# Performance work log

Measured on AMD Instinct MI355X. Metric: run time of the kernel, lower is better.

## Reference

```python
import jax, jax.numpy as jnp
import numpy as np

N_NODES = 50000
N_EDGES = 800000
N_GRAPHS = 64
IN_CH = 128
HID = [64, 128]
MLP_CH = [128, 64, 64, 64, 1]


def _glorot(key, fan_in, fan_out):
    lim = jnp.sqrt(6.0 / (fan_in + fan_out))
    return jax.random.uniform(key, (fan_in, fan_out), jnp.float32, -lim, lim)


def setup_inputs() -> dict:
    key = jax.random.key(0)
    ks = jax.random.split(key, 16)
    x = jax.random.normal(ks[0], (N_NODES, IN_CH), jnp.float32)
    edge_index = jax.random.randint(ks[1], (2, N_EDGES), 0, N_NODES, jnp.int64)
    batch = jnp.sort(jax.random.randint(ks[2], (N_NODES,), 0, N_GRAPHS, jnp.int64))
    inp = {"x": x, "edge_index": edge_index, "batch": batch}
    # GCNConv weights (x @ W + b)
    inp["W1"] = _glorot(ks[3], IN_CH, HID[0]);  inp["b1"] = jnp.zeros((HID[0],), jnp.float32)
    inp["W2"] = _glorot(ks[4], HID[0], HID[1]); inp["b2"] = jnp.zeros((HID[1],), jnp.float32)
    # MLP weights
    for i in range(4):
        inp[f"M{i+1}"] = _glorot(ks[5 + i], MLP_CH[i], MLP_CH[i + 1])
        inp[f"c{i+1}"] = jnp.zeros((MLP_CH[i + 1],), jnp.float32)
    return inp


def _gcn_conv(x, src, dst, dinv, W, b):
    # x' = D^-1/2 (A + I) D^-1/2 (x W) + b, via gather-scale-scatter over edges
    h = x @ W                                   # [N, F]
    norm = dinv[src] * dinv[dst]                # [E+N]
    msg = h[src] * norm[:, None]                # gather + scale
    out = jax.ops.segment_sum(msg, dst, num_segments=x.shape[0])
    return out + b


def reference(x, edge_index, batch, W1, b1, W2, b2, M1, c1, M2, c2, M3, c3, M4, c4):
    N = x.shape[0]
    x = x.astype(jnp.float32)
    # add self loops (PyG GCNConv default)
    loops = jnp.arange(N, dtype=edge_index.dtype)
    src = jnp.concatenate([edge_index[0], loops])
    dst = jnp.concatenate([edge_index[1], loops])
    deg = jax.ops.segment_sum(jnp.ones_like(src, jnp.float32), dst, num_segments=N)
    dinv = jnp.where(deg > 0, jax.lax.rsqrt(jnp.maximum(deg, 1.0)), 0.0)

    h = jax.nn.relu(_gcn_conv(x, src, dst, dinv, W1, b1))
    h = jax.nn.relu(_gcn_conv(h, src, dst, dinv, W2, b2))

    # global mean pool per graph
    sums = jax.ops.segment_sum(h, batch, num_segments=N_GRAPHS)
    cnts = jax.ops.segment_sum(jnp.ones((N,), jnp.float32), batch, num_segments=N_GRAPHS)
    g = sums / jnp.maximum(cnts, 1.0)[:, None]   # [G, 128]

    # MLP (eval mode: dropout is identity)
    g = jax.nn.leaky_relu(g @ M1 + c1, negative_slope=0.2)
    g = jax.nn.leaky_relu(g @ M2 + c2, negative_slope=0.1)
    g = jax.nn.leaky_relu(g @ M3 + c3, negative_slope=0.1)
    g = jax.nn.relu(g @ M4 + c4)
    return g
```

## Files before the change

kernel.cpp:

```cpp
#include <hip/hip_runtime.h>
#include <hip/hip_fp16.h>

#define N_NODES 50000
#define N_EDGES 800000
#define N_GRAPHS 64

#define CAP 64
#define FILL_STRIPES 256

struct __align__(8)  h4v { __half2 a, b; };
struct __align__(16) h8v { __half2 a, b, c, d; };


__global__ void k_zero_pack(int* __restrict__ cnt, float* __restrict__ sums,
                            const int* __restrict__ src, const int* __restrict__ dst,
                            unsigned* __restrict__ pk,
                            const float* __restrict__ W2, __half* __restrict__ w2h,
                            const int* __restrict__ batch, int* __restrict__ gend) {
    int i = blockIdx.x * 256 + threadIdx.x;
    if (i < N_NODES) {
        cnt[i] = 0;
        if (i == N_NODES - 1 || batch[i] != batch[i + 1]) gend[batch[i]] = i + 1;
    }
    if (i < N_GRAPHS * 128) sums[i] = 0.f;
    if (i < 64 * 128) w2h[i] = __float2half_rn(W2[i]);
    if (i < N_EDGES) pk[i] = ((unsigned)dst[i] << 16) | (unsigned)src[i];
}


__global__ void k_fill_direct(const unsigned* __restrict__ pk, int* __restrict__ cnt,
                              unsigned short* __restrict__ csr, int E) {
    const int range = blockIdx.x & 7;
    const int stripe = blockIdx.x >> 3;
    const unsigned lo = range * (N_NODES / 8);
    const unsigned hi = lo + (N_NODES / 8);
    for (int e = stripe * 256 + threadIdx.x; e < E; e += FILL_STRIPES * 256) {
        unsigned p = pk[e];
        unsigned d = p >> 16;
        if (d >= lo && d < hi) {
            int slot = atomicAdd(&cnt[d], 1);
            if (slot < CAP) csr[(size_t)d * CAP + slot] = (unsigned short)(p & 0xffffu);
        }
    }
}


__global__ __launch_bounds__(256) void k_gemm1(const float* __restrict__ A,
                                               const float* __restrict__ W,
                                               const int* __restrict__ cnt,
                                               __half* __restrict__ Cout, int N) {
    const int FIN = 128;
    __shared__ __align__(16) float As[64 * (FIN + 2)];
    __shared__ __align__(16) float Wsm[FIN * 64];
    const int t = threadIdx.x;
    const int row0 = blockIdx.x * 64;

    const int NF4 = 64 * FIN / 4;
    for (int idx = t; idx < NF4; idx += 256) {
        int r = idx / (FIN / 4);
        int c4 = idx % (FIN / 4);
        float4 v = make_float4(0.f, 0.f, 0.f, 0.f);
        if (row0 + r < N) v = ((const float4*)(A + (size_t)(row0 + r) * FIN))[c4];
        float* p = &As[r * (FIN + 2) + c4 * 4];
        ((float2*)p)[0] = make_float2(v.x, v.y);
        ((float2*)p)[1] = make_float2(v.z, v.w);
    }
    for (int idx = t; idx < FIN * 16; idx += 256) {
        int r = idx / 16, c4 = idx % 16;
        *((float4*)&Wsm[r * 64 + c4 * 4]) = ((const float4*)(W + (size_t)r * 64))[c4];
    }
    __syncthreads();

    const int tc = (t & 15) * 4;
    const int tr = (t >> 4) * 4;
    float acc[4][4] = {};
#pragma unroll 4
    for (int k = 0; k < FIN; k += 2) {
        float2 a[4];
#pragma unroll
        for (int r = 0; r < 4; ++r)
            a[r] = *(const float2*)&As[(tr + r) * (FIN + 2) + k];
        float4 w0 = *(const float4*)&Wsm[k * 64 + tc];
        float4 w1 = *(const float4*)&Wsm[(k + 1) * 64 + tc];
#pragma unroll
        for (int r = 0; r < 4; ++r) {
            acc[r][0] = fmaf(a[r].x, w0.x, acc[r][0]);
            acc[r][1] = fmaf(a[r].x, w0.y, acc[r][1]);
            acc[r][2] = fmaf(a[r].x, w0.z, acc[r][2]);
            acc[r][3] = fmaf(a[r].x, w0.w, acc[r][3]);
            acc[r][0] = fmaf(a[r].y, w1.x, acc[r][0]);
            acc[r][1] = fmaf(a[r].y, w1.y, acc[r][1]);
            acc[r][2] = fmaf(a[r].y, w1.z, acc[r][2]);
            acc[r][3] = fmaf(a[r].y, w1.w, acc[r][3]);
        }
    }

#pragma unroll
    for (int r = 0; r < 4; ++r) {
        int row = row0 + tr + r;
        if (row < N) {
            float s = rsqrtf((float)(min(cnt[row], CAP) + 1));
            __half2* dsth = (__half2*)(Cout + (size_t)row * 64 + tc);
            dsth[0] = __floats2half2_rn(acc[r][0] * s, acc[r][1] * s);
            dsth[1] = __floats2half2_rn(acc[r][2] * s, acc[r][3] * s);
        }
    }
}


template <bool RELU>
__global__ void k_agg(const h8v* __restrict__ h, const int* __restrict__ cnt,
                      const unsigned short* __restrict__ csr,
                      const float* __restrict__ bias, h8v* __restrict__ out, int N) {
    int node = blockIdx.x * 32 + (threadIdx.x >> 3);
    int lane = threadIdx.x & 7;
    if (node >= N) return;
    int c = min(cnt[node], CAP);
    float di = rsqrtf((float)(c + 1));
    h8v sv = h[(size_t)node * 8 + lane];
    float2 p0 = __half22float2(sv.a), p1 = __half22float2(sv.b);
    float2 p2 = __half22float2(sv.c), p3 = __half22float2(sv.d);
    float f0 = p0.x, f1 = p0.y, f2 = p1.x, f3 = p1.y;
    float f4 = p2.x, f5 = p2.y, f6 = p3.x, f7 = p3.y;
    float g0 = 0, g1 = 0, g2 = 0, g3 = 0, g4 = 0, g5 = 0, g6 = 0, g7 = 0;
    const unsigned short* row = csr + (size_t)node * CAP;
    int j = 0;
    for (; j + 4 <= c; j += 4) {
        ushort4 s4 = *(const ushort4*)(row + j);
        h8v v0 = h[(size_t)s4.x * 8 + lane];
        h8v v1 = h[(size_t)s4.y * 8 + lane];
        h8v v2 = h[(size_t)s4.z * 8 + lane];
        h8v v3 = h[(size_t)s4.w * 8 + lane];
        float2 a0 = __half22float2(v0.a), a1 = __half22float2(v0.b),
               a2 = __half22float2(v0.c), a3 = __half22float2(v0.d);
        float2 b0 = __half22float2(v1.a), b1 = __half22float2(v1.b),
               b2 = __half22float2(v1.c), b3 = __half22float2(v1.d);
        f0 += a0.x; f1 += a0.y; f2 += a1.x; f3 += a1.y;
        f4 += a2.x; f5 += a2.y; f6 += a3.x; f7 += a3.y;
        g0 += b0.x; g1 += b0.y; g2 += b1.x; g3 += b1.y;
        g4 += b2.x; g5 += b2.y; g6 += b3.x; g7 += b3.y;
        float2 c0 = __half22float2(v2.a), c1 = __half22float2(v2.b),
               c2 = __half22float2(v2.c), c3 = __half22float2(v2.d);
        float2 d0 = __half22float2(v3.a), d1 = __half22float2(v3.b),
               d2 = __half22float2(v3.c), d3 = __half22float2(v3.d);
        f0 += c0.x; f1 += c0.y; f2 += c1.x; f3 += c1.y;
        f4 += c2.x; f5 += c2.y; f6 += c3.x; f7 += c3.y;
        g0 += d0.x; g1 += d0.y; g2 += d1.x; g3 += d1.y;
        g4 += d2.x; g5 += d2.y; g6 += d3.x; g7 += d3.y;
    }
    for (; j < c; ++j) {
        h8v v = h[(size_t)row[j] * 8 + lane];
        float2 a0 = __half22float2(v.a), a1 = __half22float2(v.b),
               a2 = __half22float2(v.c), a3 = __half22float2(v.d);
        f0 += a0.x; f1 += a0.y; f2 += a1.x; f3 += a1.y;
        f4 += a2.x; f5 += a2.y; f6 += a3.x; f7 += a3.y;
    }
    float s0 = f0 + g0, s1 = f1 + g1, s2 = f2 + g2, s3 = f3 + g3;
    float s4 = f4 + g4, s5 = f5 + g5, s6 = f6 + g6, s7 = f7 + g7;
    h8v o;
    if (RELU) {
        float4 bv0 = ((const float4*)bias)[lane * 2];
        float4 bv1 = ((const float4*)bias)[lane * 2 + 1];
        float r0 = fmaf(s0, di, bv0.x); r0 = r0 > 0.f ? r0 : 0.f;
        float r1 = fmaf(s1, di, bv0.y); r1 = r1 > 0.f ? r1 : 0.f;
        float r2 = fmaf(s2, di, bv0.z); r2 = r2 > 0.f ? r2 : 0.f;
        float r3 = fmaf(s3, di, bv0.w); r3 = r3 > 0.f ? r3 : 0.f;
        float r4 = fmaf(s4, di, bv1.x); r4 = r4 > 0.f ? r4 : 0.f;
        float r5 = fmaf(s5, di, bv1.y); r5 = r5 > 0.f ? r5 : 0.f;
        float r6 = fmaf(s6, di, bv1.z); r6 = r6 > 0.f ? r6 : 0.f;
        float r7 = fmaf(s7, di, bv1.w); r7 = r7 > 0.f ? r7 : 0.f;
        o.a = __floats2half2_rn(di * r0, di * r1);
        o.b = __floats2half2_rn(di * r2, di * r3);
        o.c = __floats2half2_rn(di * r4, di * r5);
        o.d = __floats2half2_rn(di * r6, di * r7);
    } else {
        o.a = __floats2half2_rn(s0 * di, s1 * di);
        o.b = __floats2half2_rn(s2 * di, s3 * di);
        o.c = __floats2half2_rn(s4 * di, s5 * di);
        o.d = __floats2half2_rn(s6 * di, s7 * di);
    }
    out[(size_t)node * 8 + lane] = o;
}


__global__ __launch_bounds__(256) void k_gemm_pool128(
    const __half2* __restrict__ A2,
    const __half2* __restrict__ w2h,
    const float* __restrict__ bias,
    const int* __restrict__ batch,
    float* __restrict__ sums, int N) {
    __shared__ __align__(16) float As[64 * 66];
    __shared__ __align__(16) __half2 Wh[64 * 64];
    __shared__ float red[8][132];
    __shared__ int batchLDS[64];
    const int t = threadIdx.x;
    const int row0 = blockIdx.x * 64;

    for (int idx = t; idx < 4096; idx += 256) Wh[idx] = w2h[idx];
    if (t < 64) batchLDS[t] = batch[min(row0 + t, N - 1)];
    for (int idx = t; idx < 64 * 32; idx += 256) {
        int r = idx >> 5, c2 = idx & 31;
        float2 v = make_float2(0.f, 0.f);
        if (row0 + r < N) v = __half22float2(A2[(size_t)(row0 + r) * 32 + c2]);
        *(float2*)&As[r * 66 + c2 * 2] = v;
    }
    __syncthreads();

    const int tc = (t & 31) * 4;
    const int tr = (t >> 5) * 8;
    float acc[8][4] = {};
#pragma unroll 4
    for (int k = 0; k < 64; k += 2) {
        float2 a[8];
#pragma unroll
        for (int r = 0; r < 8; ++r)
            a[r] = *(const float2*)&As[(tr + r) * 66 + k];
        h4v wv0 = *(const h4v*)&Wh[k * 64 + (tc >> 1)];
        h4v wv1 = *(const h4v*)&Wh[(k + 1) * 64 + (tc >> 1)];
        float2 w00 = __half22float2(wv0.a), w01 = __half22float2(wv0.b);
        float2 w10 = __half22float2(wv1.a), w11 = __half22float2(wv1.b);
#pragma unroll
        for (int r = 0; r < 8; ++r) {
            acc[r][0] = fmaf(a[r].x, w00.x, acc[r][0]);
            acc[r][1] = fmaf(a[r].x, w00.y, acc[r][1]);
            acc[r][2] = fmaf(a[r].x, w01.x, acc[r][2]);
            acc[r][3] = fmaf(a[r].x, w01.y, acc[r][3]);
            acc[r][0] = fmaf(a[r].y, w10.x, acc[r][0]);
            acc[r][1] = fmaf(a[r].y, w10.y, acc[r][1]);
            acc[r][2] = fmaf(a[r].y, w11.x, acc[r][2]);
            acc[r][3] = fmaf(a[r].y, w11.y, acc[r][3]);
        }
    }

    float4 bv = *(const float4*)&bias[tc];
    float v[8][4];
#pragma unroll
    for (int r = 0; r < 8; ++r) {
        bool valid = (row0 + tr + r) < N;
        v[r][0] = valid ? fmaxf(acc[r][0] + bv.x, 0.f) : 0.f;
        v[r][1] = valid ? fmaxf(acc[r][1] + bv.y, 0.f) : 0.f;
        v[r][2] = valid ? fmaxf(acc[r][2] + bv.z, 0.f) : 0.f;
        v[r][3] = valid ? fmaxf(acc[r][3] + bv.w, 0.f) : 0.f;
    }

    const int g0 = batchLDS[0], g1 = batchLDS[63];
    const int rg = t >> 5;
    for (int g = g0; g <= g1; ++g) {
        float p0 = 0.f, p1 = 0.f, p2 = 0.f, p3 = 0.f;
#pragma unroll
        for (int r = 0; r < 8; ++r) {
            if (batchLDS[tr + r] == g) { p0 += v[r][0]; p1 += v[r][1]; p2 += v[r][2]; p3 += v[r][3]; }
        }
        red[rg][tc + 0] = p0; red[rg][tc + 1] = p1;
        red[rg][tc + 2] = p2; red[rg][tc + 3] = p3;
        __syncthreads();
        for (int off = 4; off > 0; off >>= 1) {
            if (rg < off) {
#pragma unroll
                for (int c = 0; c < 4; ++c) red[rg][tc + c] += red[rg + off][tc + c];
            }
            __syncthreads();
        }
        if (rg == 0) {
#pragma unroll
            for (int c = 0; c < 4; ++c)
                atomicAdd(&sums[g * 128 + tc + c], red[0][tc + c]);
        }
        __syncthreads();
    }
}


__global__ void k_mlp(const float* __restrict__ sums, const int* __restrict__ gend,
                      const float* __restrict__ M1, const float* __restrict__ c1,
                      const float* __restrict__ M2, const float* __restrict__ c2,
                      const float* __restrict__ M3, const float* __restrict__ c3,
                      const float* __restrict__ M4, const float* __restrict__ c4,
                      float* __restrict__ out) {
    __shared__ float g[128], t1[64], t2[64], t3[64];
    __shared__ float cntb;
    int b = blockIdx.x;
    int t = threadIdx.x;
    if (t == 0) {
        int lb = (b > 0) ? gend[b - 1] : 0;
        cntb = fmaxf((float)(gend[b] - lb), 1.0f);
    }
    __syncthreads();
    if (t < 128) g[t] = sums[b * 128 + t] / cntb;
    __syncthreads();
    if (t < 64) {
        float acc = c1[t];
        for (int k = 0; k < 128; ++k) acc = fmaf(g[k], M1[k * 64 + t], acc);
        t1[t] = acc >= 0.f ? acc : 0.2f * acc;
    }
    __syncthreads();
    if (t < 64) {
        float acc = c2[t];
        for (int k = 0; k < 64; ++k) acc = fmaf(t1[k], M2[k * 64 + t], acc);
        t2[t] = acc >= 0.f ? acc : 0.1f * acc;
    }
    __syncthreads();
    if (t < 64) {
        float acc = c3[t];
        for (int k = 0; k < 64; ++k) acc = fmaf(t2[k], M3[k * 64 + t], acc);
        t3[t] = acc >= 0.f ? acc : 0.1f * acc;
    }
    __syncthreads();
    if (t == 0) {
        float acc = c4[0];
        for (int k = 0; k < 64; ++k) acc = fmaf(t3[k], M4[k], acc);
        out[b] = fmaxf(acc, 0.f);
    }
}


extern "C" void kernel_launch(void* const* d_in, const int* in_sizes, int n_in,
                              void* d_out, int out_size, void* d_ws, size_t ws_size,
                              hipStream_t stream) {
    const float* x   = (const float*)d_in[0];
    const int*   ei  = (const int*)d_in[1];
    const int*   bat = (const int*)d_in[2];
    const float* W1  = (const float*)d_in[3];
    const float* b1  = (const float*)d_in[4];
    const float* W2  = (const float*)d_in[5];
    const float* b2  = (const float*)d_in[6];
    const float* M1  = (const float*)d_in[7];
    const float* c1  = (const float*)d_in[8];
    const float* M2  = (const float*)d_in[9];
    const float* c2  = (const float*)d_in[10];
    const float* M3  = (const float*)d_in[11];
    const float* c3  = (const float*)d_in[12];
    const float* M4  = (const float*)d_in[13];
    const float* c4  = (const float*)d_in[14];
    float* out = (float*)d_out;

    const int* src = ei;
    const int* dst = ei + N_EDGES;

    float* bufA    = (float*)d_ws;
    float* bufB    = bufA + (size_t)N_NODES * 64;
    float* sums    = bufB + (size_t)N_NODES * 64;
    int*   cnt     = (int*)(sums + N_GRAPHS * 128);
    unsigned short* csr = (unsigned short*)(cnt + N_NODES);
    unsigned* pk   = (unsigned*)(csr + (size_t)N_NODES * CAP);
    __half* w2h    = (__half*)(pk + N_EDGES);
    int*   gend    = (int*)(w2h + 64 * 128);

    k_zero_pack<<<(N_EDGES + 255) / 256, 256, 0, stream>>>(cnt, sums, src, dst, pk,
                                                           W2, w2h, bat, gend);
    k_fill_direct<<<8 * FILL_STRIPES, 256, 0, stream>>>(pk, cnt, csr, N_EDGES);

    const int NBLK = (N_NODES + 63) / 64;
    const int ABLK = (N_NODES + 31) / 32;

    k_gemm1<<<NBLK, 256, 0, stream>>>(x, W1, cnt, (__half*)bufA, N_NODES);
    k_agg<true><<<ABLK, 256, 0, stream>>>(
        (const h8v*)bufA, cnt, csr, b1, (h8v*)bufB, N_NODES);

    k_agg<false><<<ABLK, 256, 0, stream>>>(
        (const h8v*)bufB, cnt, csr, nullptr, (h8v*)bufA, N_NODES);
    k_gemm_pool128<<<NBLK, 256, 0, stream>>>(
        (const __half2*)bufA, (const __half2*)w2h, b2, bat, sums, N_NODES);

    k_mlp<<<N_GRAPHS, 128, 0, stream>>>(sums, gend,
                                        M1, c1, M2, c2, M3, c3, M4, c4, out);
}
```

Measured before the change: 217.0 us.

## Merge build and tail stages into cooperative kernels with grid syncs

Replaces the zero/pack and fill kernels with one cooperative kernel that zeroes counters, syncs the grid, then fills the CSR directly from src/dst without the packed edge array. The second aggregation, the GEMM-pool and the MLP are merged into one cooperative persistent kernel with grid-wide syncs between phases. This aims to cut kernel launch gaps and the extra pack pass, in exchange for grid-sync cost, fewer resident blocks and less parallelism in some phases. The tail kernel's shared-memory use may limit how many blocks can be co-resident.

New measurement: 520.8 us. +140.0%, slower.

```diff
diff --git a/kernel.cpp b/kernel.cpp
--- a/kernel.cpp
+++ b/kernel.cpp
@@ -1,45 +1,46 @@
 #include <hip/hip_runtime.h>
 #include <hip/hip_fp16.h>
+#include <hip/hip_cooperative_groups.h>
+
+namespace cg = cooperative_groups;
 
 #define N_NODES 50000
 #define N_EDGES 800000
 #define N_GRAPHS 64
 
 #define CAP 64
-#define FILL_STRIPES 256
+#define BUILD_BLOCKS 1024
+#define TAIL_BLOCKS 1024
 
 struct __align__(8)  h4v { __half2 a, b; };
 struct __align__(16) h8v { __half2 a, b, c, d; };
 
 
-__global__ void k_zero_pack(int* __restrict__ cnt, float* __restrict__ sums,
-                            const int* __restrict__ src, const int* __restrict__ dst,
-                            unsigned* __restrict__ pk,
-                            const float* __restrict__ W2, __half* __restrict__ w2h,
-                            const int* __restrict__ batch, int* __restrict__ gend) {
-    int i = blockIdx.x * 256 + threadIdx.x;
-    if (i < N_NODES) {
-        cnt[i] = 0;
-        if (i == N_NODES - 1 || batch[i] != batch[i + 1]) gend[batch[i]] = i + 1;
-    }
-    if (i < N_GRAPHS * 128) sums[i] = 0.f;
-    if (i < 64 * 128) w2h[i] = __float2half_rn(W2[i]);
-    if (i < N_EDGES) pk[i] = ((unsigned)dst[i] << 16) | (unsigned)src[i];
-}
-
-
-__global__ void k_fill_direct(const unsigned* __restrict__ pk, int* __restrict__ cnt,
-                              unsigned short* __restrict__ csr, int E) {
+__global__ __launch_bounds__(256, 4) void k_build(
+    const int* __restrict__ src, const int* __restrict__ dst,
+    int* __restrict__ cnt, float* __restrict__ sums,
+    const float* __restrict__ W2, __half* __restrict__ w2h,
+    const int* __restrict__ batch, int* __restrict__ gend,
+    unsigned short* __restrict__ csr) {
+    const int tid = blockIdx.x * 256 + threadIdx.x;
+    if (tid < N_NODES) {
+        cnt[tid] = 0;
+        if (tid == N_NODES - 1 || batch[tid] != batch[tid + 1]) gend[batch[tid]] = tid + 1;
+    }
+    if (tid < N_GRAPHS * 128) sums[tid] = 0.f;
+    if (tid < 64 * 128) w2h[tid] = __float2half_rn(W2[tid]);
+
+    cg::this_grid().sync();
+
     const int range = blockIdx.x & 7;
     const int stripe = blockIdx.x >> 3;
-    const unsigned lo = range * (N_NODES / 8);
-    const unsigned hi = lo + (N_NODES / 8);
-    for (int e = stripe * 256 + threadIdx.x; e < E; e += FILL_STRIPES * 256) {
-        unsigned p = pk[e];
-        unsigned d = p >> 16;
+    const int lo = range * (N_NODES / 8);
+    const int hi = lo + (N_NODES / 8);
+    for (int e = stripe * 256 + threadIdx.x; e < N_EDGES; e += (BUILD_BLOCKS / 8) * 256) {
+        int d = dst[e];
         if (d >= lo && d < hi) {
             int slot = atomicAdd(&cnt[d], 1);
-            if (slot < CAP) csr[(size_t)d * CAP + slot] = (unsigned short)(p & 0xffffu);
+            if (slot < CAP) csr[(size_t)d * CAP + slot] = (unsigned short)src[e];
         }
     }
 }
@@ -108,22 +109,11 @@
 }
 
 
-template <bool RELU>
-__global__ void k_agg(const h8v* __restrict__ h, const int* __restrict__ cnt,
-                      const unsigned short* __restrict__ csr,
-                      const float* __restrict__ bias, h8v* __restrict__ out, int N) {
-    int node = blockIdx.x * 32 + (threadIdx.x >> 3);
-    int lane = threadIdx.x & 7;
-    if (node >= N) return;
-    int c = min(cnt[node], CAP);
-    float di = rsqrtf((float)(c + 1));
-    h8v sv = h[(size_t)node * 8 + lane];
-    float2 p0 = __half22float2(sv.a), p1 = __half22float2(sv.b);
-    float2 p2 = __half22float2(sv.c), p3 = __half22float2(sv.d);
-    float f0 = p0.x, f1 = p0.y, f2 = p1.x, f3 = p1.y;
-    float f4 = p2.x, f5 = p2.y, f6 = p3.x, f7 = p3.y;
+__device__ __forceinline__ void gather_node(const h8v* __restrict__ h,
+                                            const unsigned short* __restrict__ row,
+                                            int c, int lane,
+                                            float* f ) {
     float g0 = 0, g1 = 0, g2 = 0, g3 = 0, g4 = 0, g5 = 0, g6 = 0, g7 = 0;
-    const unsigned short* row = csr + (size_t)node * CAP;
     int j = 0;
     for (; j + 4 <= c; j += 4) {
         ushort4 s4 = *(const ushort4*)(row + j);
@@ -135,16 +125,16 @@
                a2 = __half22float2(v0.c), a3 = __half22float2(v0.d);
         float2 b0 = __half22float2(v1.a), b1 = __half22float2(v1.b),
                b2 = __half22float2(v1.c), b3 = __half22float2(v1.d);
-        f0 += a0.x; f1 += a0.y; f2 += a1.x; f3 += a1.y;
-        f4 += a2.x; f5 += a2.y; f6 += a3.x; f7 += a3.y;
+        f[0] += a0.x; f[1] += a0.y; f[2] += a1.x; f[3] += a1.y;
+        f[4] += a2.x; f[5] += a2.y; f[6] += a3.x; f[7] += a3.y;
         g0 += b0.x; g1 += b0.y; g2 += b1.x; g3 += b1.y;
         g4 += b2.x; g5 += b2.y; g6 += b3.x; g7 += b3.y;
         float2 c0 = __half22float2(v2.a), c1 = __half22float2(v2.b),
                c2 = __half22float2(v2.c), c3 = __half22float2(v2.d);
         float2 d0 = __half22float2(v3.a), d1 = __half22float2(v3.b),
                d2 = __half22float2(v3.c), d3 = __half22float2(v3.d);
-        f0 += c0.x; f1 += c0.y; f2 += c1.x; f3 += c1.y;
-        f4 += c2.x; f5 += c2.y; f6 += c3.x; f7 += c3.y;
+        f[0] += c0.x; f[1] += c0.y; f[2] += c1.x; f[3] += c1.y;
+        f[4] += c2.x; f[5] += c2.y; f[6] += c3.x; f[7] += c3.y;
         g0 += d0.x; g1 += d0.y; g2 += d1.x; g3 += d1.y;
         g4 += d2.x; g5 += d2.y; g6 += d3.x; g7 += d3.y;
     }
@@ -152,164 +142,206 @@
         h8v v = h[(size_t)row[j] * 8 + lane];
         float2 a0 = __half22float2(v.a), a1 = __half22float2(v.b),
                a2 = __half22float2(v.c), a3 = __half22float2(v.d);
-        f0 += a0.x; f1 += a0.y; f2 += a1.x; f3 += a1.y;
-        f4 += a2.x; f5 += a2.y; f6 += a3.x; f7 += a3.y;
-    }
-    float s0 = f0 + g0, s1 = f1 + g1, s2 = f2 + g2, s3 = f3 + g3;
-    float s4 = f4 + g4, s5 = f5 + g5, s6 = f6 + g6, s7 = f7 + g7;
+        f[0] += a0.x; f[1] += a0.y; f[2] += a1.x; f[3] += a1.y;
+        f[4] += a2.x; f[5] += a2.y; f[6] += a3.x; f[7] += a3.y;
+    }
+    f[0] += g0; f[1] += g1; f[2] += g2; f[3] += g3;
+    f[4] += g4; f[5] += g5; f[6] += g6; f[7] += g7;
+}
+
+
+__global__ void k_agg1(const h8v* __restrict__ h, const int* __restrict__ cnt,
+                       const unsigned short* __restrict__ csr,
+                       const float* __restrict__ bias, h8v* __restrict__ out, int N) {
+    int node = blockIdx.x * 32 + (threadIdx.x >> 3);
+    int lane = threadIdx.x & 7;
+    if (node >= N) return;
+    int c = min(cnt[node], CAP);
+    float di = rsqrtf((float)(c + 1));
+    h8v sv = h[(size_t)node * 8 + lane];
+    float2 p0 = __half22float2(sv.a), p1 = __half22float2(sv.b);
+    float2 p2 = __half22float2(sv.c), p3 = __half22float2(sv.d);
+    float f[8] = {p0.x, p0.y, p1.x, p1.y, p2.x, p2.y, p3.x, p3.y};
+    gather_node(h, csr + (size_t)node * CAP, c, lane, f);
+    float4 bv0 = ((const float4*)bias)[lane * 2];
+    float4 bv1 = ((const float4*)bias)[lane * 2 + 1];
+    float r0 = fmaf(f[0], di, bv0.x); r0 = r0 > 0.f ? r0 : 0.f;
+    float r1 = fmaf(f[1], di, bv0.y); r1 = r1 > 0.f ? r1 : 0.f;
+    float r2 = fmaf(f[2], di, bv0.z); r2 = r2 > 0.f ? r2 : 0.f;
+    float r3 = fmaf(f[3], di, bv0.w); r3 = r3 > 0.f ? r3 : 0.f;
+    float r4 = fmaf(f[4], di, bv1.x); r4 = r4 > 0.f ? r4 : 0.f;
+    float r5 = fmaf(f[5], di, bv1.y); r5 = r5 > 0.f ? r5 : 0.f;
+    float r6 = fmaf(f[6], di, bv1.z); r6 = r6 > 0.f ? r6 : 0.f;
+    float r7 = fmaf(f[7], di, bv1.w); r7 = r7 > 0.f ? r7 : 0.f;
     h8v o;
-    if (RELU) {
-        float4 bv0 = ((const float4*)bias)[lane * 2];
-        float4 bv1 = ((const float4*)bias)[lane * 2 + 1];
-        float r0 = fmaf(s0, di, bv0.x); r0 = r0 > 0.f ? r0 : 0.f;
-        float r1 = fmaf(s1, di, bv0.y); r1 = r1 > 0.f ? r1 : 0.f;
-        float r2 = fmaf(s2, di, bv0.z); r2 = r2 > 0.f ? r2 : 0.f;
-        float r3 = fmaf(s3, di, bv0.w); r3 = r3 > 0.f ? r3 : 0.f;
-        float r4 = fmaf(s4, di, bv1.x); r4 = r4 > 0.f ? r4 : 0.f;
-        float r5 = fmaf(s5, di, bv1.y); r5 = r5 > 0.f ? r5 : 0.f;
-        float r6 = fmaf(s6, di, bv1.z); r6 = r6 > 0.f ? r6 : 0.f;
-        float r7 = fmaf(s7, di, bv1.w); r7 = r7 > 0.f ? r7 : 0.f;
-        o.a = __floats2half2_rn(di * r0, di * r1);
-        o.b = __floats2half2_rn(di * r2, di * r3);
-        o.c = __floats2half2_rn(di * r4, di * r5);
-        o.d = __floats2half2_rn(di * r6, di * r7);
-    } else {
-        o.a = __floats2half2_rn(s0 * di, s1 * di);
-        o.b = __floats2half2_rn(s2 * di, s3 * di);
-        o.c = __floats2half2_rn(s4 * di, s5 * di);
-        o.d = __floats2half2_rn(s6 * di, s7 * di);
-    }
+    o.a = __floats2half2_rn(di * r0, di * r1);
+    o.b = __floats2half2_rn(di * r2, di * r3);
+    o.c = __floats2half2_rn(di * r4, di * r5);
+    o.d = __floats2half2_rn(di * r6, di * r7);
     out[(size_t)node * 8 + lane] = o;
 }
 
 
-__global__ __launch_bounds__(256) void k_gemm_pool128(
-    const __half2* __restrict__ A2,
+__global__ __launch_bounds__(256, 4) void k_tail(
+    const h8v* __restrict__ hB,
+    const int* __restrict__ cnt,
+    const unsigned short* __restrict__ csr,
+    h8v* __restrict__ zA,
     const __half2* __restrict__ w2h,
-    const float* __restrict__ bias,
+    const float* __restrict__ b2,
     const int* __restrict__ batch,
-    float* __restrict__ sums, int N) {
+    float* __restrict__ sums,
+    const int* __restrict__ gend,
+    const float* __restrict__ M1, const float* __restrict__ c1,
+    const float* __restrict__ M2, const float* __restrict__ c2,
+    const float* __restrict__ M3, const float* __restrict__ c3,
+    const float* __restrict__ M4, const float* __restrict__ c4,
+    float* __restrict__ out) {
     __shared__ __align__(16) float As[64 * 66];
     __shared__ __align__(16) __half2 Wh[64 * 64];
     __shared__ float red[8][132];
     __shared__ int batchLDS[64];
+    __shared__ float gv[128], t1[64], t2[64], t3[64];
+    __shared__ float cntb;
     const int t = threadIdx.x;
-    const int row0 = blockIdx.x * 64;
-
-    for (int idx = t; idx < 4096; idx += 256) Wh[idx] = w2h[idx];
-    if (t < 64) batchLDS[t] = batch[min(row0 + t, N - 1)];
-    for (int idx = t; idx < 64 * 32; idx += 256) {
-        int r = idx >> 5, c2 = idx & 31;
-        float2 v = make_float2(0.f, 0.f);
-        if (row0 + r < N) v = __half22float2(A2[(size_t)(row0 + r) * 32 + c2]);
-        *(float2*)&As[r * 66 + c2 * 2] = v;
-    }
-    __syncthreads();
-
-    const int tc = (t & 31) * 4;
-    const int tr = (t >> 5) * 8;
-    float acc[8][4] = {};
+    const int N = N_NODES;
+
+    {
+        const int lane = t & 7;
+        const int grp = t >> 3;
+        for (int base = blockIdx.x * 32; base < N; base += TAIL_BLOCKS * 32) {
+            int node = base + grp;
+            if (node < N) {
+                int c = min(cnt[node], CAP);
+                float di = rsqrtf((float)(c + 1));
+                h8v sv = hB[(size_t)node * 8 + lane];
+                float2 p0 = __half22float2(sv.a), p1 = __half22float2(sv.b);
+                float2 p2 = __half22float2(sv.c), p3 = __half22float2(sv.d);
+                float f[8] = {p0.x, p0.y, p1.x, p1.y, p2.x, p2.y, p3.x, p3.y};
+                gather_node(hB, csr + (size_t)node * CAP, c, lane, f);
+                h8v o;
+                o.a = __floats2half2_rn(f[0] * di, f[1] * di);
+                o.b = __floats2half2_rn(f[2] * di, f[3] * di);
+                o.c = __floats2half2_rn(f[4] * di, f[5] * di);
+                o.d = __floats2half2_rn(f[6] * di, f[7] * di);
+                zA[(size_t)node * 8 + lane] = o;
+            }
+        }
+    }
+
+    cg::this_grid().sync();
+
+    const __half2* A2 = (const __half2*)zA;
+    for (int row0 = blockIdx.x * 64; row0 < N; row0 += TAIL_BLOCKS * 64) {
+        for (int idx = t; idx < 4096; idx += 256) Wh[idx] = w2h[idx];
+        if (t < 64) batchLDS[t] = batch[min(row0 + t, N - 1)];
+        for (int idx = t; idx < 64 * 32; idx += 256) {
+            int r = idx >> 5, c2 = idx & 31;
+            float2 v = make_float2(0.f, 0.f);
+            if (row0 + r < N) v = __half22float2(A2[(size_t)(row0 + r) * 32 + c2]);
+            *(float2*)&As[r * 66 + c2 * 2] = v;
+        }
+        __syncthreads();
+
+        const int tc = (t & 31) * 4;
+        const int tr = (t >> 5) * 8;
+        float acc[8][4] = {};
 #pragma unroll 4
-    for (int k = 0; k < 64; k += 2) {
-        float2 a[8];
-#pragma unroll
-        for (int r = 0; r < 8; ++r)
-            a[r] = *(const float2*)&As[(tr + r) * 66 + k];
-        h4v wv0 = *(const h4v*)&Wh[k * 64 + (tc >> 1)];
-        h4v wv1 = *(const h4v*)&Wh[(k + 1) * 64 + (tc >> 1)];
-        float2 w00 = __half22float2(wv0.a), w01 = __half22float2(wv0.b);
-        float2 w10 = __half22float2(wv1.a), w11 = __half22float2(wv1.b);
+        for (int k = 0; k < 64; k += 2) {
+            float2 a[8];
+#pragma unroll
+            for (int r = 0; r < 8; ++r)
+                a[r] = *(const float2*)&As[(tr + r) * 66 + k];
+            h4v wv0 = *(const h4v*)&Wh[k * 64 + (tc >> 1)];
+            h4v wv1 = *(const h4v*)&Wh[(k + 1) * 64 + (tc >> 1)];
+            float2 w00 = __half22float2(wv0.a), w01 = __half22float2(wv0.b);
+            float2 w10 = __half22float2(wv1.a), w11 = __half22float2(wv1.b);
+#pragma unroll
+            for (int r = 0; r < 8; ++r) {
+                acc[r][0] = fmaf(a[r].x, w00.x, acc[r][0]);
+                acc[r][1] = fmaf(a[r].x, w00.y, acc[r][1]);
+                acc[r][2] = fmaf(a[r].x, w01.x, acc[r][2]);
+                acc[r][3] = fmaf(a[r].x, w01.y, acc[r][3]);
+                acc[r][0] = fmaf(a[r].y, w10.x, acc[r][0]);
+                acc[r][1] = fmaf(a[r].y, w10.y, acc[r][1]);
+                acc[r][2] = fmaf(a[r].y, w11.x, acc[r][2]);
+                acc[r][3] = fmaf(a[r].y, w11.y, acc[r][3]);
+            }
+        }
+
+        float4 bv = *(const float4*)&b2[tc];
+        float v[8][4];
 #pragma unroll
         for (int r = 0; r < 8; ++r) {
-            acc[r][0] = fmaf(a[r].x, w00.x, acc[r][0]);
-            acc[r][1] = fmaf(a[r].x, w00.y, acc[r][1]);
-            acc[r][2] = fmaf(a[r].x, w01.x, acc[r][2]);
-            acc[r][3] = fmaf(a[r].x, w01.y, acc[r][3]);
-            acc[r][0] = fmaf(a[r].y, w10.x, acc[r][0]);
-            acc[r][1] = fmaf(a[r].y, w10.y, acc[r][1]);
-            acc[r][2] = fmaf(a[r].y, w11.x, acc[r][2]);
-            acc[r][3] = fmaf(a[r].y, w11.y, acc[r][3]);
-        }
-    }
-
-    float4 bv = *(const float4*)&bias[tc];
-    float v[8][4];
-#pragma unroll
-    for (int r = 0; r < 8; ++r) {
-        bool valid = (row0 + tr + r) < N;
-        v[r][0] = valid ? fmaxf(acc[r][0] + bv.x, 0.f) : 0.f;
-        v[r][1] = valid ? fmaxf(acc[r][1] + bv.y, 0.f) : 0.f;
-        v[r][2] = valid ? fmaxf(acc[r][2] + bv.z, 0.f) : 0.f;
-        v[r][3] = valid ? fmaxf(acc[r][3] + bv.w, 0.f) : 0.f;
-    }
-
-    const int g0 = batchLDS[0], g1 = batchLDS[63];
-    const int rg = t >> 5;
-    for (int g = g0; g <= g1; ++g) {
-        float p0 = 0.f, p1 = 0.f, p2 = 0.f, p3 = 0.f;
-#pragma unroll
-        for (int r = 0; r < 8; ++r) {
-            if (batchLDS[tr + r] == g) { p0 += v[r][0]; p1 += v[r][1]; p2 += v[r][2]; p3 += v[r][3]; }
-        }
-        red[rg][tc + 0] = p0; red[rg][tc + 1] = p1;
-        red[rg][tc + 2] = p2; red[rg][tc + 3] = p3;
-        __syncthreads();
-        for (int off = 4; off > 0; off >>= 1) {
-            if (rg < off) {
-#pragma unroll
-                for (int c = 0; c < 4; ++c) red[rg][tc + c] += red[rg + off][tc + c];
+            bool valid = (row0 + tr + r) < N;
+            v[r][0] = valid ? fmaxf(acc[r][0] + bv.x, 0.f) : 0.f;
+            v[r][1] = valid ? fmaxf(acc[r][1] + bv.y, 0.f) : 0.f;
+            v[r][2] = valid ? fmaxf(acc[r][2] + bv.z, 0.f) : 0.f;
+            v[r][3] = valid ? fmaxf(acc[r][3] + bv.w, 0.f) : 0.f;
+        }
+
+        const int g0 = batchLDS[0], g1 = batchLDS[63];
+        const int rg = t >> 5;
+        for (int g = g0; g <= g1; ++g) {
+            float p0 = 0.f, p1 = 0.f, p2 = 0.f, p3 = 0.f;
+#pragma unroll
+            for (int r = 0; r < 8; ++r) {
+                if (batchLDS[tr + r] == g) { p0 += v[r][0]; p1 += v[r][1]; p2 += v[r][2]; p3 += v[r][3]; }
+            }
+            red[rg][tc + 0] = p0; red[rg][tc + 1] = p1;
+            red[rg][tc + 2] = p2; red[rg][tc + 3] = p3;
+            __syncthreads();
+            for (int off = 4; off > 0; off >>= 1) {
+                if (rg < off) {
+#pragma unroll
+                    for (int c = 0; c < 4; ++c) red[rg][tc + c] += red[rg + off][tc + c];
+                }
+                __syncthreads();
+            }
+            if (rg == 0) {
+#pragma unroll
+                for (int c = 0; c < 4; ++c)
+                    atomicAdd(&sums[g * 128 + tc + c], red[0][tc + c]);
             }
             __syncthreads();
         }
-        if (rg == 0) {
-#pragma unroll
-            for (int c = 0; c < 4; ++c)
-                atomicAdd(&sums[g * 128 + tc + c], red[0][tc + c]);
-        }
-        __syncthreads();
-    }
-}
-
-
-__global__ void k_mlp(const float* __restrict__ sums, const int* __restrict__ gend,
-                      const float* __restrict__ M1, const float* __restrict__ c1,
-                      const float* __restrict__ M2, const float* __restrict__ c2,
-                      const float* __restrict__ M3, const float* __restrict__ c3,
-                      const float* __restrict__ M4, const float* __restrict__ c4,
-                      float* __restrict__ out) {
-    __shared__ float g[128], t1[64], t2[64], t3[64];
-    __shared__ float cntb;
-    int b = blockIdx.x;
-    int t = threadIdx.x;
-    if (t == 0) {
-        int lb = (b > 0) ? gend[b - 1] : 0;
-        cntb = fmaxf((float)(gend[b] - lb), 1.0f);
-    }
-    __syncthreads();
-    if (t < 128) g[t] = sums[b * 128 + t] / cntb;
-    __syncthreads();
-    if (t < 64) {
-        float acc = c1[t];
-        for (int k = 0; k < 128; ++k) acc = fmaf(g[k], M1[k * 64 + t], acc);
-        t1[t] = acc >= 0.f ? acc : 0.2f * acc;
-    }
-    __syncthreads();
-    if (t < 64) {
-        float acc = c2[t];
-        for (int k = 0; k < 64; ++k) acc = fmaf(t1[k], M2[k * 64 + t], acc);
-        t2[t] = acc >= 0.f ? acc : 0.1f * acc;
-    }
-    __syncthreads();
-    if (t < 64) {
-        float acc = c3[t];
-        for (int k = 0; k < 64; ++k) acc = fmaf(t2[k], M3[k * 64 + t], acc);
-        t3[t] = acc >= 0.f ? acc : 0.1f * acc;
-    }
-    __syncthreads();
-    if (t == 0) {
-        float acc = c4[0];
-        for (int k = 0; k < 64; ++k) acc = fmaf(t3[k], M4[k], acc);
-        out[b] = fmaxf(acc, 0.f);
+        __syncthreads();
+    }
+
+    cg::this_grid().sync();
+
+    if (blockIdx.x < N_GRAPHS) {
+        int b = blockIdx.x;
+        if (t == 0) {
+            int lb = (b > 0) ? gend[b - 1] : 0;
+            cntb = fmaxf((float)(gend[b] - lb), 1.0f);
+        }
+        __syncthreads();
+        if (t < 128) gv[t] = sums[b * 128 + t] / cntb;
+        __syncthreads();
+        if (t < 64) {
+            float acc = c1[t];
+            for (int k = 0; k < 128; ++k) acc = fmaf(gv[k], M1[k * 64 + t], acc);
+            t1[t] = acc >= 0.f ? acc : 0.2f * acc;
+        }
+        __syncthreads();
+        if (t < 64) {
+            float acc = c2[t];
+            for (int k = 0; k < 64; ++k) acc = fmaf(t1[k], M2[k * 64 + t], acc);
+            t2[t] = acc >= 0.f ? acc : 0.1f * acc;
+        }
+        __syncthreads();
+        if (t < 64) {
+            float acc = c3[t];
+            for (int k = 0; k < 64; ++k) acc = fmaf(t2[k], M3[k * 64 + t], acc);
+            t3[t] = acc >= 0.f ? acc : 0.1f * acc;
+        }
+        __syncthreads();
+        if (t == 0) {
+            float acc = c4[0];
+            for (int k = 0; k < 64; ++k) acc = fmaf(t3[k], M4[k], acc);
+            out[b] = fmaxf(acc, 0.f);
+        }
     }
 }
 
@@ -342,26 +374,32 @@
     float* sums    = bufB + (size_t)N_NODES * 64;
     int*   cnt     = (int*)(sums + N_GRAPHS * 128);
     unsigned short* csr = (unsigned short*)(cnt + N_NODES);
-    unsigned* pk   = (unsigned*)(csr + (size_t)N_NODES * CAP);
-    __half* w2h    = (__half*)(pk + N_EDGES);
+    __half* w2h    = (__half*)(csr + (size_t)N_NODES * CAP);
     int*   gend    = (int*)(w2h + 64 * 128);
 
-    k_zero_pack<<<(N_EDGES + 255) / 256, 256, 0, stream>>>(cnt, sums, src, dst, pk,
-                                                           W2, w2h, bat, gend);
-    k_fill_direct<<<8 * FILL_STRIPES, 256, 0, stream>>>(pk, cnt, csr, N_EDGES);
+    {
+        void* args[] = {(void*)&src, (void*)&dst, (void*)&cnt, (void*)&sums,
+                        (void*)&W2, (void*)&w2h, (void*)&bat, (void*)&gend, (void*)&csr};
+        hipLaunchCooperativeKernel((const void*)k_build, dim3(BUILD_BLOCKS), dim3(256),
+                                   args, 0, stream);
+    }
 
     const int NBLK = (N_NODES + 63) / 64;
     const int ABLK = (N_NODES + 31) / 32;
 
     k_gemm1<<<NBLK, 256, 0, stream>>>(x, W1, cnt, (__half*)bufA, N_NODES);
-    k_agg<true><<<ABLK, 256, 0, stream>>>(
+    k_agg1<<<ABLK, 256, 0, stream>>>(
         (const h8v*)bufA, cnt, csr, b1, (h8v*)bufB, N_NODES);
 
-    k_agg<false><<<ABLK, 256, 0, stream>>>(
-        (const h8v*)bufB, cnt, csr, nullptr, (h8v*)bufA, N_NODES);
-    k_gemm_pool128<<<NBLK, 256, 0, stream>>>(
-        (const __half2*)bufA, (const __half2*)w2h, b2, bat, sums, N_NODES);
-
-    k_mlp<<<N_GRAPHS, 128, 0, stream>>>(sums, gend,
-                                        M1, c1, M2, c2, M3, c3, M4, c4, out);
-}
+    {
+        const h8v* hB = (const h8v*)bufB;
+        h8v* zA = (h8v*)bufA;
+        const __half2* w2h2 = (const __half2*)w2h;
+        void* args[] = {(void*)&hB, (void*)&cnt, (void*)&csr, (void*)&zA, (void*)&w2h2,
+                        (void*)&b2, (void*)&bat, (void*)&sums, (void*)&gend,
+                        (void*)&M1, (void*)&c1, (void*)&M2, (void*)&c2,
+                        (void*)&M3, (void*)&c3, (void*)&M4, (void*)&c4, (void*)&out};
+        hipLaunchCooperativeKernel((const void*)k_tail, dim3(TAIL_BLOCKS), dim3(256),
+                                   args, 0, stream);
+    }
+}
```

## Fuse MLP into pooling kernel via last-block pattern and drop edge packing

Applied to the files above, without the earlier changes.

The separate edge-packing pass is removed: the fill kernel now reads src/dst directly instead of a packed 32-bit array, and the init kernel shrinks to node-sized launches. The MLP kernel is folded into the pooling GEMM kernel: each block increments a done counter, and the last block to finish runs the four-layer MLP for all 64 graphs using a tiled register GEMM. This removes one launch plus the pack kernel's reads and writes, but fill reads two arrays per edge and the MLP runs serially on a single block at the tail.

Result: slower. 287.5 us (+32.4%).

```diff
diff --git a/kernel.cpp b/kernel.cpp
--- a/kernel.cpp
+++ b/kernel.cpp
@@ -12,34 +12,32 @@
 struct __align__(16) h8v { __half2 a, b, c, d; };
 
 
-__global__ void k_zero_pack(int* __restrict__ cnt, float* __restrict__ sums,
-                            const int* __restrict__ src, const int* __restrict__ dst,
-                            unsigned* __restrict__ pk,
-                            const float* __restrict__ W2, __half* __restrict__ w2h,
-                            const int* __restrict__ batch, int* __restrict__ gend) {
+__global__ void k_init(int* __restrict__ cnt, float* __restrict__ sums,
+                       const float* __restrict__ W2, __half* __restrict__ w2h,
+                       const int* __restrict__ batch, int* __restrict__ gend,
+                       int* __restrict__ done) {
     int i = blockIdx.x * 256 + threadIdx.x;
+    if (i == 0) *done = 0;
     if (i < N_NODES) {
         cnt[i] = 0;
         if (i == N_NODES - 1 || batch[i] != batch[i + 1]) gend[batch[i]] = i + 1;
     }
     if (i < N_GRAPHS * 128) sums[i] = 0.f;
     if (i < 64 * 128) w2h[i] = __float2half_rn(W2[i]);
-    if (i < N_EDGES) pk[i] = ((unsigned)dst[i] << 16) | (unsigned)src[i];
-}
-
-
-__global__ void k_fill_direct(const unsigned* __restrict__ pk, int* __restrict__ cnt,
-                              unsigned short* __restrict__ csr, int E) {
+}
+
+
+__global__ void k_fill_direct(const int* __restrict__ src, const int* __restrict__ dst,
+                              int* __restrict__ cnt, unsigned short* __restrict__ csr, int E) {
     const int range = blockIdx.x & 7;
     const int stripe = blockIdx.x >> 3;
-    const unsigned lo = range * (N_NODES / 8);
-    const unsigned hi = lo + (N_NODES / 8);
+    const int lo = range * (N_NODES / 8);
+    const int hi = lo + (N_NODES / 8);
     for (int e = stripe * 256 + threadIdx.x; e < E; e += FILL_STRIPES * 256) {
-        unsigned p = pk[e];
-        unsigned d = p >> 16;
+        int d = dst[e];
         if (d >= lo && d < hi) {
             int slot = atomicAdd(&cnt[d], 1);
-            if (slot < CAP) csr[(size_t)d * CAP + slot] = (unsigned short)(p & 0xffffu);
+            if (slot < CAP) csr[(size_t)d * CAP + slot] = (unsigned short)src[e];
         }
     }
 }
@@ -188,11 +186,19 @@
     const __half2* __restrict__ w2h,
     const float* __restrict__ bias,
     const int* __restrict__ batch,
-    float* __restrict__ sums, int N) {
-    __shared__ __align__(16) float As[64 * 66];
-    __shared__ __align__(16) __half2 Wh[64 * 64];
+    float* __restrict__ sums, int N,
+    int* __restrict__ done, const int* __restrict__ gend,
+    const float* __restrict__ M1, const float* __restrict__ c1,
+    const float* __restrict__ M2, const float* __restrict__ c2,
+    const float* __restrict__ M3, const float* __restrict__ c3,
+    const float* __restrict__ M4, const float* __restrict__ c4,
+    float* __restrict__ out) {
+    __shared__ __align__(16) unsigned char smem[33280];
     __shared__ float red[8][132];
     __shared__ int batchLDS[64];
+    __shared__ bool amLast;
+    float* As = (float*)smem;
+    __half2* Wh = (__half2*)(smem + 16896);
     const int t = threadIdx.x;
     const int row0 = blockIdx.x * 64;
 
@@ -208,108 +214,176 @@
 
     const int tc = (t & 31) * 4;
     const int tr = (t >> 5) * 8;
-    float acc[8][4] = {};
+    {
+        float acc[8][4] = {};
 #pragma unroll 4
-    for (int k = 0; k < 64; k += 2) {
-        float2 a[8];
-#pragma unroll
-        for (int r = 0; r < 8; ++r)
-            a[r] = *(const float2*)&As[(tr + r) * 66 + k];
-        h4v wv0 = *(const h4v*)&Wh[k * 64 + (tc >> 1)];
-        h4v wv1 = *(const h4v*)&Wh[(k + 1) * 64 + (tc >> 1)];
-        float2 w00 = __half22float2(wv0.a), w01 = __half22float2(wv0.b);
-        float2 w10 = __half22float2(wv1.a), w11 = __half22float2(wv1.b);
+        for (int k = 0; k < 64; k += 2) {
+            float2 a[8];
+#pragma unroll
+            for (int r = 0; r < 8; ++r)
+                a[r] = *(const float2*)&As[(tr + r) * 66 + k];
+            h4v wv0 = *(const h4v*)&Wh[k * 64 + (tc >> 1)];
+            h4v wv1 = *(const h4v*)&Wh[(k + 1) * 64 + (tc >> 1)];
+            float2 w00 = __half22float2(wv0.a), w01 = __half22float2(wv0.b);
+            float2 w10 = __half22float2(wv1.a), w11 = __half22float2(wv1.b);
+#pragma unroll
+            for (int r = 0; r < 8; ++r) {
+                acc[r][0] = fmaf(a[r].x, w00.x, acc[r][0]);
+                acc[r][1] = fmaf(a[r].x, w00.y, acc[r][1]);
+                acc[r][2] = fmaf(a[r].x, w01.x, acc[r][2]);
+                acc[r][3] = fmaf(a[r].x, w01.y, acc[r][3]);
+                acc[r][0] = fmaf(a[r].y, w10.x, acc[r][0]);
+                acc[r][1] = fmaf(a[r].y, w10.y, acc[r][1]);
+                acc[r][2] = fmaf(a[r].y, w11.x, acc[r][2]);
+                acc[r][3] = fmaf(a[r].y, w11.y, acc[r][3]);
+            }
+        }
+
+        float4 bv = *(const float4*)&bias[tc];
+        float v[8][4];
 #pragma unroll
         for (int r = 0; r < 8; ++r) {
-            acc[r][0] = fmaf(a[r].x, w00.x, acc[r][0]);
-            acc[r][1] = fmaf(a[r].x, w00.y, acc[r][1]);
-            acc[r][2] = fmaf(a[r].x, w01.x, acc[r][2]);
-            acc[r][3] = fmaf(a[r].x, w01.y, acc[r][3]);
-            acc[r][0] = fmaf(a[r].y, w10.x, acc[r][0]);
-            acc[r][1] = fmaf(a[r].y, w10.y, acc[r][1]);
-            acc[r][2] = fmaf(a[r].y, w11.x, acc[r][2]);
-            acc[r][3] = fmaf(a[r].y, w11.y, acc[r][3]);
-        }
-    }
-
-    float4 bv = *(const float4*)&bias[tc];
-    float v[8][4];
-#pragma unroll
-    for (int r = 0; r < 8; ++r) {
-        bool valid = (row0 + tr + r) < N;
-        v[r][0] = valid ? fmaxf(acc[r][0] + bv.x, 0.f) : 0.f;
-        v[r][1] = valid ? fmaxf(acc[r][1] + bv.y, 0.f) : 0.f;
-        v[r][2] = valid ? fmaxf(acc[r][2] + bv.z, 0.f) : 0.f;
-        v[r][3] = valid ? fmaxf(acc[r][3] + bv.w, 0.f) : 0.f;
-    }
-
-    const int g0 = batchLDS[0], g1 = batchLDS[63];
-    const int rg = t >> 5;
-    for (int g = g0; g <= g1; ++g) {
-        float p0 = 0.f, p1 = 0.f, p2 = 0.f, p3 = 0.f;
-#pragma unroll
-        for (int r = 0; r < 8; ++r) {
-            if (batchLDS[tr + r] == g) { p0 += v[r][0]; p1 += v[r][1]; p2 += v[r][2]; p3 += v[r][3]; }
-        }
-        red[rg][tc + 0] = p0; red[rg][tc + 1] = p1;
-        red[rg][tc + 2] = p2; red[rg][tc + 3] = p3;
-        __syncthreads();
-        for (int off = 4; off > 0; off >>= 1) {
-            if (rg < off) {
-#pragma unroll
-                for (int c = 0; c < 4; ++c) red[rg][tc + c] += red[rg + off][tc + c];
+            bool valid = (row0 + tr + r) < N;
+            v[r][0] = valid ? fmaxf(acc[r][0] + bv.x, 0.f) : 0.f;
+            v[r][1] = valid ? fmaxf(acc[r][1] + bv.y, 0.f) : 0.f;
+            v[r][2] = valid ? fmaxf(acc[r][2] + bv.z, 0.f) : 0.f;
+            v[r][3] = valid ? fmaxf(acc[r][3] + bv.w, 0.f) : 0.f;
+        }
+
+        const int g0 = batchLDS[0], g1 = batchLDS[63];
+        const int rg = t >> 5;
+        for (int g = g0; g <= g1; ++g) {
+            float p0 = 0.f, p1 = 0.f, p2 = 0.f, p3 = 0.f;
+#pragma unroll
+            for (int r = 0; r < 8; ++r) {
+                if (batchLDS[tr + r] == g) { p0 += v[r][0]; p1 += v[r][1]; p2 += v[r][2]; p3 += v[r][3]; }
+            }
+            red[rg][tc + 0] = p0; red[rg][tc + 1] = p1;
+            red[rg][tc + 2] = p2; red[rg][tc + 3] = p3;
+            __syncthreads();
+            for (int off = 4; off > 0; off >>= 1) {
+                if (rg < off) {
+#pragma unroll
+                    for (int c = 0; c < 4; ++c) red[rg][tc + c] += red[rg + off][tc + c];
+                }
+                __syncthreads();
+            }
+            if (rg == 0) {
+#pragma unroll
+                for (int c = 0; c < 4; ++c)
+                    atomicAdd(&sums[g * 128 + tc + c], red[0][tc + c]);
             }
             __syncthreads();
         }
-        if (rg == 0) {
-#pragma unroll
-            for (int c = 0; c < 4; ++c)
-                atomicAdd(&sums[g * 128 + tc + c], red[0][tc + c]);
-        }
+    }
+
+    __threadfence();
+    __syncthreads();
+    if (t == 0) amLast = (atomicAdd(done, 1) == (int)gridDim.x - 1);
+    __syncthreads();
+    if (!amLast) return;
+    __threadfence();
+
+    float* G = (float*)smem;
+    for (int idx = t; idx < N_GRAPHS * 128; idx += 256) {
+        int g = idx >> 7;
+        int lb = (g > 0) ? gend[g - 1] : 0;
+        float cg = fmaxf((float)(gend[g] - lb), 1.0f);
+        G[idx] = atomicAdd(&sums[idx], 0.f) / cg;
+    }
+    __syncthreads();
+
+    const int mc = (t & 15) * 4;
+    const int mr = (t >> 4) * 4;
+    float* T1 = (float*)smem;
+    float* T2 = (float*)(smem + 16384);
+    {
+        float acc[4][4] = {};
+        for (int k = 0; k < 128; ++k) {
+            float4 w = *(const float4*)&M1[k * 64 + mc];
+            float a0 = G[(mr + 0) * 128 + k], a1 = G[(mr + 1) * 128 + k];
+            float a2 = G[(mr + 2) * 128 + k], a3 = G[(mr + 3) * 128 + k];
+            acc[0][0] = fmaf(a0, w.x, acc[0][0]); acc[0][1] = fmaf(a0, w.y, acc[0][1]);
+            acc[0][2] = fmaf(a0, w.z, acc[0][2]); acc[0][3] = fmaf(a0, w.w, acc[0][3]);
+            acc[1][0] = fmaf(a1, w.x, acc[1][0]); acc[1][1] = fmaf(a1, w.y, acc[1][1]);
+            acc[1][2] = fmaf(a1, w.z, acc[1][2]); acc[1][3] = fmaf(a1, w.w, acc[1][3]);
+            acc[2][0] = fmaf(a2, w.x, acc[2][0]); acc[2][1] = fmaf(a2, w.y, acc[2][1]);
+            acc[2][2] = fmaf(a2, w.z, acc[2][2]); acc[2][3] = fmaf(a2, w.w, acc[2][3]);
+            acc[3][0] = fmaf(a3, w.x, acc[3][0]); acc[3][1] = fmaf(a3, w.y, acc[3][1]);
+            acc[3][2] = fmaf(a3, w.z, acc[3][2]); acc[3][3] = fmaf(a3, w.w, acc[3][3]);
+        }
+        float4 cv = *(const float4*)&c1[mc];
         __syncthreads();
-    }
-}
-
-
-__global__ void k_mlp(const float* __restrict__ sums, const int* __restrict__ gend,
-                      const float* __restrict__ M1, const float* __restrict__ c1,
-                      const float* __restrict__ M2, const float* __restrict__ c2,
-                      const float* __restrict__ M3, const float* __restrict__ c3,
-                      const float* __restrict__ M4, const float* __restrict__ c4,
-                      float* __restrict__ out) {
-    __shared__ float g[128], t1[64], t2[64], t3[64];
-    __shared__ float cntb;
-    int b = blockIdx.x;
-    int t = threadIdx.x;
-    if (t == 0) {
-        int lb = (b > 0) ? gend[b - 1] : 0;
-        cntb = fmaxf((float)(gend[b] - lb), 1.0f);
-    }
-    __syncthreads();
-    if (t < 128) g[t] = sums[b * 128 + t] / cntb;
-    __syncthreads();
-    if (t < 64) {
-        float acc = c1[t];
-        for (int k = 0; k < 128; ++k) acc = fmaf(g[k], M1[k * 64 + t], acc);
-        t1[t] = acc >= 0.f ? acc : 0.2f * acc;
-    }
-    __syncthreads();
-    if (t < 64) {
-        float acc = c2[t];
-        for (int k = 0; k < 64; ++k) acc = fmaf(t1[k], M2[k * 64 + t], acc);
-        t2[t] = acc >= 0.f ? acc : 0.1f * acc;
-    }
-    __syncthreads();
-    if (t < 64) {
-        float acc = c3[t];
-        for (int k = 0; k < 64; ++k) acc = fmaf(t2[k], M3[k * 64 + t], acc);
-        t3[t] = acc >= 0.f ? acc : 0.1f * acc;
-    }
-    __syncthreads();
-    if (t == 0) {
+#pragma unroll
+        for (int r = 0; r < 4; ++r) {
+            float o0 = acc[r][0] + cv.x, o1 = acc[r][1] + cv.y;
+            float o2 = acc[r][2] + cv.z, o3 = acc[r][3] + cv.w;
+            T1[(mr + r) * 64 + mc + 0] = o0 >= 0.f ? o0 : 0.2f * o0;
+            T1[(mr + r) * 64 + mc + 1] = o1 >= 0.f ? o1 : 0.2f * o1;
+            T1[(mr + r) * 64 + mc + 2] = o2 >= 0.f ? o2 : 0.2f * o2;
+            T1[(mr + r) * 64 + mc + 3] = o3 >= 0.f ? o3 : 0.2f * o3;
+        }
+    }
+    __syncthreads();
+    {
+        float acc[4][4] = {};
+        for (int k = 0; k < 64; ++k) {
+            float4 w = *(const float4*)&M2[k * 64 + mc];
+            float a0 = T1[(mr + 0) * 64 + k], a1 = T1[(mr + 1) * 64 + k];
+            float a2 = T1[(mr + 2) * 64 + k], a3 = T1[(mr + 3) * 64 + k];
+            acc[0][0] = fmaf(a0, w.x, acc[0][0]); acc[0][1] = fmaf(a0, w.y, acc[0][1]);
+            acc[0][2] = fmaf(a0, w.z, acc[0][2]); acc[0][3] = fmaf(a0, w.w, acc[0][3]);
+            acc[1][0] = fmaf(a1, w.x, acc[1][0]); acc[1][1] = fmaf(a1, w.y, acc[1][1]);
+            acc[1][2] = fmaf(a1, w.z, acc[1][2]); acc[1][3] = fmaf(a1, w.w, acc[1][3]);
+            acc[2][0] = fmaf(a2, w.x, acc[2][0]); acc[2][1] = fmaf(a2, w.y, acc[2][1]);
+            acc[2][2] = fmaf(a2, w.z, acc[2][2]); acc[2][3] = fmaf(a2, w.w, acc[2][3]);
+            acc[3][0] = fmaf(a3, w.x, acc[3][0]); acc[3][1] = fmaf(a3, w.y, acc[3][1]);
+            acc[3][2] = fmaf(a3, w.z, acc[3][2]); acc[3][3] = fmaf(a3, w.w, acc[3][3]);
+        }
+        float4 cv = *(const float4*)&c2[mc];
+#pragma unroll
+        for (int r = 0; r < 4; ++r) {
+            float o0 = acc[r][0] + cv.x, o1 = acc[r][1] + cv.y;
+            float o2 = acc[r][2] + cv.z, o3 = acc[r][3] + cv.w;
+            T2[(mr + r) * 64 + mc + 0] = o0 >= 0.f ? o0 : 0.1f * o0;
+            T2[(mr + r) * 64 + mc + 1] = o1 >= 0.f ? o1 : 0.1f * o1;
+            T2[(mr + r) * 64 + mc + 2] = o2 >= 0.f ? o2 : 0.1f * o2;
+            T2[(mr + r) * 64 + mc + 3] = o3 >= 0.f ? o3 : 0.1f * o3;
+        }
+    }
+    __syncthreads();
+    {
+        float acc[4][4] = {};
+        for (int k = 0; k < 64; ++k) {
+            float4 w = *(const float4*)&M3[k * 64 + mc];
+            float a0 = T2[(mr + 0) * 64 + k], a1 = T2[(mr + 1) * 64 + k];
+            float a2 = T2[(mr + 2) * 64 + k], a3 = T2[(mr + 3) * 64 + k];
+            acc[0][0] = fmaf(a0, w.x, acc[0][0]); acc[0][1] = fmaf(a0, w.y, acc[0][1]);
+            acc[0][2] = fmaf(a0, w.z, acc[0][2]); acc[0][3] = fmaf(a0, w.w, acc[0][3]);
+            acc[1][0] = fmaf(a1, w.x, acc[1][0]); acc[1][1] = fmaf(a1, w.y, acc[1][1]);
+            acc[1][2] = fmaf(a1, w.z, acc[1][2]); acc[1][3] = fmaf(a1, w.w, acc[1][3]);
+            acc[2][0] = fmaf(a2, w.x, acc[2][0]); acc[2][1] = fmaf(a2, w.y, acc[2][1]);
+            acc[2][2] = fmaf(a2, w.z, acc[2][2]); acc[2][3] = fmaf(a2, w.w, acc[2][3]);
+            acc[3][0] = fmaf(a3, w.x, acc[3][0]); acc[3][1] = fmaf(a3, w.y, acc[3][1]);
+            acc[3][2] = fmaf(a3, w.z, acc[3][2]); acc[3][3] = fmaf(a3, w.w, acc[3][3]);
+        }
+        float4 cv = *(const float4*)&c3[mc];
+        __syncthreads();
+#pragma unroll
+        for (int r = 0; r < 4; ++r) {
+            float o0 = acc[r][0] + cv.x, o1 = acc[r][1] + cv.y;
+            float o2 = acc[r][2] + cv.z, o3 = acc[r][3] + cv.w;
+            T1[(mr + r) * 64 + mc + 0] = o0 >= 0.f ? o0 : 0.1f * o0;
+            T1[(mr + r) * 64 + mc + 1] = o1 >= 0.f ? o1 : 0.1f * o1;
+            T1[(mr + r) * 64 + mc + 2] = o2 >= 0.f ? o2 : 0.1f * o2;
+            T1[(mr + r) * 64 + mc + 3] = o3 >= 0.f ? o3 : 0.1f * o3;
+        }
+    }
+    __syncthreads();
+    if (t < N_GRAPHS) {
         float acc = c4[0];
-        for (int k = 0; k < 64; ++k) acc = fmaf(t3[k], M4[k], acc);
-        out[b] = fmaxf(acc, 0.f);
+        for (int k = 0; k < 64; ++k) acc = fmaf(T1[t * 64 + k], M4[k], acc);
+        out[t] = fmaxf(acc, 0.f);
     }
 }
 
@@ -342,13 +416,12 @@
     float* sums    = bufB + (size_t)N_NODES * 64;
     int*   cnt     = (int*)(sums + N_GRAPHS * 128);
     unsigned short* csr = (unsigned short*)(cnt + N_NODES);
-    unsigned* pk   = (unsigned*)(csr + (size_t)N_NODES * CAP);
-    __half* w2h    = (__half*)(pk + N_EDGES);
+    __half* w2h    = (__half*)(csr + (size_t)N_NODES * CAP);
     int*   gend    = (int*)(w2h + 64 * 128);
-
-    k_zero_pack<<<(N_EDGES + 255) / 256, 256, 0, stream>>>(cnt, sums, src, dst, pk,
-                                                           W2, w2h, bat, gend);
-    k_fill_direct<<<8 * FILL_STRIPES, 256, 0, stream>>>(pk, cnt, csr, N_EDGES);
+    int*   done    = gend + 64;
+
+    k_init<<<(N_NODES + 255) / 256, 256, 0, stream>>>(cnt, sums, W2, w2h, bat, gend, done);
+    k_fill_direct<<<8 * FILL_STRIPES, 256, 0, stream>>>(src, dst, cnt, csr, N_EDGES);
 
     const int NBLK = (N_NODES + 63) / 64;
     const int ABLK = (N_NODES + 31) / 32;
@@ -360,8 +433,6 @@
     k_agg<false><<<ABLK, 256, 0, stream>>>(
         (const h8v*)bufB, cnt, csr, nullptr, (h8v*)bufA, N_NODES);
     k_gemm_pool128<<<NBLK, 256, 0, stream>>>(
-        (const __half2*)bufA, (const __half2*)w2h, b2, bat, sums, N_NODES);
-
-    k_mlp<<<N_GRAPHS, 128, 0, stream>>>(sums, gend,
-                                        M1, c1, M2, c2, M3, c3, M4, c4, out);
-}
+        (const __half2*)bufA, (const __half2*)w2h, b2, bat, sums, N_NODES,
+        done, gend, M1, c1, M2, c2, M3, c3, M4, c4, out);
+}
```
